# Kernel optimization log

Measured on AMD Instinct MI355X. Metric: run time of the kernel, lower is better.

The kernel has to match this reference:

```python
import jax, jax.numpy as jnp
import numpy as np

K = 3       # kernel_size
STRIDE = 1
PAD = 1


def setup_inputs() -> dict:
    key = jax.random.key(0)
    k1, k2, k3 = jax.random.split(key, 3)
    B, C, H, W = 4, 64, 224, 224
    x = jax.random.normal(k1, (B, C, H, W), dtype=jnp.float32)
    # fc = Conv2d(C, C, 1) -> ReLU -> Conv2d(C, C*K*K, 1); 1x1 convs == per-pixel matmuls
    w1 = jax.random.normal(k2, (C, C), dtype=jnp.float32) * (1.0 / np.sqrt(C))
    w2 = jax.random.normal(k3, (C * K * K, C), dtype=jnp.float32) * (1.0 / np.sqrt(C))
    return {"x": x, "w1": w1, "w2": w2}


def reference(x, w1, w2):
    # Involution-style dynamic depthwise conv:
    # out[b,c,h,w] = sum_{i,j} kern[b,c,i,j,h,w] * x_pad[b,c,h+i,w+j]
    B, C, H, W = x.shape
    # kernel generator (two 1x1 convs with ReLU in between)
    h = jax.nn.relu(jnp.einsum('bchw,oc->bohw', x, w1))
    kern = jnp.einsum('bohw,po->bphw', h, w2).reshape(B, C, K * K, H, W)
    # unfold 3x3 neighborhoods (pad=1, stride=1) -> (B, C, K*K, H, W)
    xp = jnp.pad(x, ((0, 0), (0, 0), (PAD, PAD), (PAD, PAD)))
    patches = jnp.stack(
        [xp[:, :, i:i + H, j:j + W] for i in range(K) for j in range(K)], axis=2)
    return jnp.einsum('bckhw,bckhw->bchw', kern, patches)
```

## Files before the change

### kernel.cpp

```cpp
#include <hip/hip_runtime.h>

#define HH   224
#define WW   224
#define HW_  (HH * WW)
#define TS   16
#define TSH  18
#define NPIX (TSH * TSH)
#define XSR  328

typedef __attribute__((ext_vector_type(8))) short bf16x8;
typedef __attribute__((ext_vector_type(4))) float f32x4;

static __device__ __forceinline__ unsigned short f2bf(float f) {
    unsigned u = __float_as_uint(f);
    u += 0x7FFFu + ((u >> 16) & 1u);
    return (unsigned short)(u >> 16);
}
static __device__ __forceinline__ float bf2f(unsigned short h) {
    return __uint_as_float(((unsigned)h) << 16);
}

__global__ __launch_bounds__(256) void prep_weights(
    const float* __restrict__ w1, const float* __restrict__ w2,
    unsigned short* __restrict__ wsb)
{
    const int i = blockIdx.x * 256 + threadIdx.x;
    unsigned short* w1b = wsb;
    unsigned short* w2p = wsb + 4096;
    if (i < 4096) w1b[i] = f2bf(w1[i]);
    const int c  = i >> 10;
    const int rr = (i >> 6) & 15;
    const int o  = i & 63;
    float v = (rr < 9) ? w2[(c * 9 + rr) * 64 + o] : 0.f;
    w2p[i] = f2bf(v);
}

__global__ __launch_bounds__(256, 2) void dynconv_mfma(
    const float* __restrict__ x, const unsigned short* __restrict__ wsb,
    float* __restrict__ out)
{
    __shared__ __align__(16) unsigned char lds[74752];
    unsigned short* xs  = (unsigned short*)lds;
    unsigned char*  hsb = lds + 41984;

    const unsigned char* w1b = (const unsigned char*)wsb;
    const unsigned char* w2p = (const unsigned char*)(wsb + 4096);

    const int b    = blockIdx.z;
    const int ty0  = blockIdx.y * TS;
    const int tx0  = blockIdx.x * TS;
    const int tid  = threadIdx.x;
    const int lane = tid & 63;
    const int w    = tid >> 6;
    const int tx   = lane & 15;
    const int g    = lane >> 4;

    const float* xb = x + (size_t)b * 64 * HW_;

    for (int i = tid; i < 64 * (NPIX / 2); i += 256) {
        int c  = i / 162;
        int pr = i - c * 162;
        int r  = pr / 9;
        int cp = pr - r * 9;
        int col0 = cp * 2;
        int gy  = ty0 + r - 1;
        int gx0 = tx0 + col0 - 1;
        float f0 = 0.f, f1 = 0.f;
        if ((unsigned)gy < (unsigned)HH) {
            const float* rowp = xb + c * HW_ + gy * WW;
            if ((unsigned)gx0 < (unsigned)WW)       f0 = rowp[gx0];
            if ((unsigned)(gx0 + 1) < (unsigned)WW) f1 = rowp[gx0 + 1];
        }
        unsigned pack = (unsigned)f2bf(f0) | ((unsigned)f2bf(f1) << 16);
        int p0 = r * TSH + col0;
        *(unsigned*)((unsigned char*)xs + c * 656 + p0 * 2) = pack;
    }
    __syncthreads();

    {
        bf16x8 aw1[4][2];
        #pragma unroll
        for (int mt = 0; mt < 4; ++mt) {
            #pragma unroll
            for (int kt = 0; kt < 2; ++kt)
                aw1[mt][kt] = *(const bf16x8*)(w1b + (mt * 16 + tx) * 128 + kt * 64 + g * 16);
        }
        #pragma unroll
        for (int q = 0; q < 4; ++q) {
            const int nt = w * 4 + q;
            const int center = (nt + 1) * TSH + tx + 1;
            bf16x8 bx[2];
            #pragma unroll
            for (int kt = 0; kt < 2; ++kt) {
                bf16x8 t;
                #pragma unroll
                for (int j = 0; j < 8; ++j)
                    t[j] = (short)xs[(kt * 32 + g * 8 + j) * XSR + center];
                bx[kt] = t;
            }
            const int pix = nt * 16 + tx;
            const unsigned swz = (unsigned)((tx & 7) << 4);
            #pragma unroll
            for (int mt = 0; mt < 4; ++mt) {
                f32x4 hc = {0.f, 0.f, 0.f, 0.f};
                hc = __builtin_amdgcn_mfma_f32_16x16x32_bf16(aw1[mt][0], bx[0], hc, 0, 0, 0);
                hc = __builtin_amdgcn_mfma_f32_16x16x32_bf16(aw1[mt][1], bx[1], hc, 0, 0, 0);
                unsigned lo = (unsigned)f2bf(fmaxf(hc[0], 0.f)) | ((unsigned)f2bf(fmaxf(hc[1], 0.f)) << 16);
                unsigned hi = (unsigned)f2bf(fmaxf(hc[2], 0.f)) | ((unsigned)f2bf(fmaxf(hc[3], 0.f)) << 16);
                unsigned byte = ((unsigned)(pix * 128 + mt * 32 + g * 8)) ^ swz;
                *(uint2*)(hsb + byte) = make_uint2(lo, hi);
            }
        }
    }

    bf16x8 bh0[2], bh1[2], bh2[2], bh3[2];
    {
        const unsigned swz = (unsigned)((tx & 7) << 4);
        #pragma unroll
        for (int kt = 0; kt < 2; ++kt) {
            unsigned p0 = (unsigned)(((w * 4 + 0) * 16 + tx) * 128 + kt * 64 + g * 16);
            unsigned p1 = (unsigned)(((w * 4 + 1) * 16 + tx) * 128 + kt * 64 + g * 16);
            unsigned p2 = (unsigned)(((w * 4 + 2) * 16 + tx) * 128 + kt * 64 + g * 16);
            unsigned p3 = (unsigned)(((w * 4 + 3) * 16 + tx) * 128 + kt * 64 + g * 16);
            bh0[kt] = *(const bf16x8*)(hsb + (p0 ^ swz));
            bh1[kt] = *(const bf16x8*)(hsb + (p1 ^ swz));
            bh2[kt] = *(const bf16x8*)(hsb + (p2 ^ swz));
            bh3[kt] = *(const bf16x8*)(hsb + (p3 ^ swz));
        }
    }

    int poff[4][4];
    #pragma unroll
    for (int q = 0; q < 4; ++q) {
        #pragma unroll
        for (int r = 0; r < 4; ++r) {
            int kk = g * 4 + r;
            int kv = kk < 9 ? kk : 0;
            int dy = kv / 3;
            int dx = kv - dy * 3;
            poff[q][r] = (w * 4 + q + dy) * TSH + (tx + dx);
        }
    }

    float* outp = out + (size_t)b * 64 * HW_ + (size_t)(ty0 + w * 4 + g) * WW + tx0 + tx;

    const unsigned char* w2base = w2p + tx * 128 + g * 16;
    bf16x8 na0 = *(const bf16x8*)(w2base);
    bf16x8 na1 = *(const bf16x8*)(w2base + 64);

    for (int c = 0; c < 64; ++c) {
        bf16x8 a0 = na0, a1 = na1;
        const int cn = (c < 63) ? c + 1 : 63;
        na0 = *(const bf16x8*)(w2base + cn * 2048);
        na1 = *(const bf16x8*)(w2base + cn * 2048 + 64);

        f32x4 acc0 = {0.f, 0.f, 0.f, 0.f};
        f32x4 acc1 = {0.f, 0.f, 0.f, 0.f};
        f32x4 acc2 = {0.f, 0.f, 0.f, 0.f};
        f32x4 acc3 = {0.f, 0.f, 0.f, 0.f};
        acc0 = __builtin_amdgcn_mfma_f32_16x16x32_bf16(a0, bh0[0], acc0, 0, 0, 0);
        acc1 = __builtin_amdgcn_mfma_f32_16x16x32_bf16(a0, bh1[0], acc1, 0, 0, 0);
        acc2 = __builtin_amdgcn_mfma_f32_16x16x32_bf16(a0, bh2[0], acc2, 0, 0, 0);
        acc3 = __builtin_amdgcn_mfma_f32_16x16x32_bf16(a0, bh3[0], acc3, 0, 0, 0);
        acc0 = __builtin_amdgcn_mfma_f32_16x16x32_bf16(a1, bh0[1], acc0, 0, 0, 0);
        acc1 = __builtin_amdgcn_mfma_f32_16x16x32_bf16(a1, bh1[1], acc1, 0, 0, 0);
        acc2 = __builtin_amdgcn_mfma_f32_16x16x32_bf16(a1, bh2[1], acc2, 0, 0, 0);
        acc3 = __builtin_amdgcn_mfma_f32_16x16x32_bf16(a1, bh3[1], acc3, 0, 0, 0);

        const unsigned short* xc = xs + c * XSR;
        float part0 = 0.f, part1 = 0.f, part2 = 0.f, part3 = 0.f;
        #pragma unroll
        for (int r = 0; r < 4; ++r) {
            part0 = fmaf(acc0[r], bf2f(xc[poff[0][r]]), part0);
            part1 = fmaf(acc1[r], bf2f(xc[poff[1][r]]), part1);
            part2 = fmaf(acc2[r], bf2f(xc[poff[2][r]]), part2);
            part3 = fmaf(acc3[r], bf2f(xc[poff[3][r]]), part3);
        }
        part0 += __shfl_xor(part0, 16, 64); part0 += __shfl_xor(part0, 32, 64);
        part1 += __shfl_xor(part1, 16, 64); part1 += __shfl_xor(part1, 32, 64);
        part2 += __shfl_xor(part2, 16, 64); part2 += __shfl_xor(part2, 32, 64);
        part3 += __shfl_xor(part3, 16, 64); part3 += __shfl_xor(part3, 32, 64);

        float v = part0;
        v = (g == 1) ? part1 : v;
        v = (g == 2) ? part2 : v;
        v = (g == 3) ? part3 : v;
        outp[(size_t)c * HW_] = v;
    }
}

extern "C" void kernel_launch(void* const* d_in, const int* in_sizes, int n_in,
                              void* d_out, int out_size, void* d_ws, size_t ws_size,
                              hipStream_t stream) {
    (void)in_sizes; (void)n_in; (void)out_size; (void)ws_size;
    const float* x  = (const float*)d_in[0];
    const float* w1 = (const float*)d_in[1];
    const float* w2 = (const float*)d_in[2];
    float* out = (float*)d_out;
    unsigned short* wsb = (unsigned short*)d_ws;

    prep_weights<<<256, 256, 0, stream>>>(w1, w2, wsb);

    dim3 grid(WW / TS, HH / TS, 4);
    dynconv_mfma<<<grid, 256, 0, stream>>>(x, wsb, out);
}
```

Before: 213.9 us.

## Keep hidden activations in registers via 16x16x16 MFMA and pixel-major LDS layout

```diff
diff --git a/kernel.cpp b/kernel.cpp
--- a/kernel.cpp
+++ b/kernel.cpp
@@ -6,9 +6,10 @@
 #define TS   16
 #define TSH  18
 #define NPIX (TSH * TSH)
-#define XSR  328
+#define XROW 144
 
 typedef __attribute__((ext_vector_type(8))) short bf16x8;
+typedef __attribute__((ext_vector_type(4))) short bf16x4;
 typedef __attribute__((ext_vector_type(4))) float f32x4;
 
 static __device__ __forceinline__ unsigned short f2bf(float f) {
@@ -35,13 +36,11 @@
     w2p[i] = f2bf(v);
 }
 
-__global__ __launch_bounds__(256, 2) void dynconv_mfma(
+__global__ __launch_bounds__(256, 3) void dynconv_mfma16(
     const float* __restrict__ x, const unsigned short* __restrict__ wsb,
     float* __restrict__ out)
 {
-    __shared__ __align__(16) unsigned char lds[74752];
-    unsigned short* xs  = (unsigned short*)lds;
-    unsigned char*  hsb = lds + 41984;
+    __shared__ __align__(16) unsigned char xsb[NPIX * XROW];
 
     const unsigned char* w1b = (const unsigned char*)wsb;
     const unsigned char* w2p = (const unsigned char*)(wsb + 4096);
@@ -57,81 +56,54 @@
 
     const float* xb = x + (size_t)b * 64 * HW_;
 
-    for (int i = tid; i < 64 * (NPIX / 2); i += 256) {
-        int c  = i / 162;
-        int pr = i - c * 162;
-        int r  = pr / 9;
-        int cp = pr - r * 9;
-        int col0 = cp * 2;
+    for (int i = tid; i < 32 * NPIX; i += 256) {
+        int cp  = i / NPIX;
+        int pix = i - cp * NPIX;
+        int r   = pix / TSH;
+        int col = pix - r * TSH;
         int gy  = ty0 + r - 1;
-        int gx0 = tx0 + col0 - 1;
+        int gx  = tx0 + col - 1;
         float f0 = 0.f, f1 = 0.f;
-        if ((unsigned)gy < (unsigned)HH) {
-            const float* rowp = xb + c * HW_ + gy * WW;
-            if ((unsigned)gx0 < (unsigned)WW)       f0 = rowp[gx0];
-            if ((unsigned)(gx0 + 1) < (unsigned)WW) f1 = rowp[gx0 + 1];
+        if ((unsigned)gy < (unsigned)HH && (unsigned)gx < (unsigned)WW) {
+            const float* p = xb + (size_t)(2 * cp) * HW_ + gy * WW + gx;
+            f0 = p[0];
+            f1 = p[HW_];
         }
-        unsigned pack = (unsigned)f2bf(f0) | ((unsigned)f2bf(f1) << 16);
-        int p0 = r * TSH + col0;
-        *(unsigned*)((unsigned char*)xs + c * 656 + p0 * 2) = pack;
+        unsigned pk = (unsigned)f2bf(f0) | ((unsigned)f2bf(f1) << 16);
+        *(unsigned*)(xsb + pix * XROW + cp * 4) = pk;
     }
     __syncthreads();
 
+    bf16x4 bq[4][4];
     {
         bf16x8 aw1[4][2];
         #pragma unroll
-        for (int mt = 0; mt < 4; ++mt) {
+        for (int mt = 0; mt < 4; ++mt)
             #pragma unroll
             for (int kt = 0; kt < 2; ++kt)
                 aw1[mt][kt] = *(const bf16x8*)(w1b + (mt * 16 + tx) * 128 + kt * 64 + g * 16);
-        }
         #pragma unroll
         for (int q = 0; q < 4; ++q) {
-            const int nt = w * 4 + q;
-            const int center = (nt + 1) * TSH + tx + 1;
-            bf16x8 bx[2];
-            #pragma unroll
-            for (int kt = 0; kt < 2; ++kt) {
-                bf16x8 t;
-                #pragma unroll
-                for (int j = 0; j < 8; ++j)
-                    t[j] = (short)xs[(kt * 32 + g * 8 + j) * XSR + center];
-                bx[kt] = t;
-            }
-            const int pix = nt * 16 + tx;
-            const unsigned swz = (unsigned)((tx & 7) << 4);
+            const int center = (w * 4 + q + 1) * TSH + (tx + 1);
+            bf16x8 bx0 = *(const bf16x8*)(xsb + center * XROW + g * 16);
+            bf16x8 bx1 = *(const bf16x8*)(xsb + center * XROW + 64 + g * 16);
             #pragma unroll
             for (int mt = 0; mt < 4; ++mt) {
                 f32x4 hc = {0.f, 0.f, 0.f, 0.f};
-                hc = __builtin_amdgcn_mfma_f32_16x16x32_bf16(aw1[mt][0], bx[0], hc, 0, 0, 0);
-                hc = __builtin_amdgcn_mfma_f32_16x16x32_bf16(aw1[mt][1], bx[1], hc, 0, 0, 0);
+                hc = __builtin_amdgcn_mfma_f32_16x16x32_bf16(aw1[mt][0], bx0, hc, 0, 0, 0);
+                hc = __builtin_amdgcn_mfma_f32_16x16x32_bf16(aw1[mt][1], bx1, hc, 0, 0, 0);
                 unsigned lo = (unsigned)f2bf(fmaxf(hc[0], 0.f)) | ((unsigned)f2bf(fmaxf(hc[1], 0.f)) << 16);
                 unsigned hi = (unsigned)f2bf(fmaxf(hc[2], 0.f)) | ((unsigned)f2bf(fmaxf(hc[3], 0.f)) << 16);
-                unsigned byte = ((unsigned)(pix * 128 + mt * 32 + g * 8)) ^ swz;
-                *(uint2*)(hsb + byte) = make_uint2(lo, hi);
+                union { uint2 u; bf16x4 v; } cv;
+                cv.u = make_uint2(lo, hi);
+                bq[q][mt] = cv.v;
             }
-        }
-    }
-
-    bf16x8 bh0[2], bh1[2], bh2[2], bh3[2];
-    {
-        const unsigned swz = (unsigned)((tx & 7) << 4);
-        #pragma unroll
-        for (int kt = 0; kt < 2; ++kt) {
-            unsigned p0 = (unsigned)(((w * 4 + 0) * 16 + tx) * 128 + kt * 64 + g * 16);
-            unsigned p1 = (unsigned)(((w * 4 + 1) * 16 + tx) * 128 + kt * 64 + g * 16);
-            unsigned p2 = (unsigned)(((w * 4 + 2) * 16 + tx) * 128 + kt * 64 + g * 16);
-            unsigned p3 = (unsigned)(((w * 4 + 3) * 16 + tx) * 128 + kt * 64 + g * 16);
-            bh0[kt] = *(const bf16x8*)(hsb + (p0 ^ swz));
-            bh1[kt] = *(const bf16x8*)(hsb + (p1 ^ swz));
-            bh2[kt] = *(const bf16x8*)(hsb + (p2 ^ swz));
-            bh3[kt] = *(const bf16x8*)(hsb + (p3 ^ swz));
         }
     }
 
     int poff[4][4];
     #pragma unroll
-    for (int q = 0; q < 4; ++q) {
+    for (int q = 0; q < 4; ++q)
         #pragma unroll
         for (int r = 0; r < 4; ++r) {
             int kk = g * 4 + r;
@@ -140,52 +112,71 @@
             int dx = kv - dy * 3;
             poff[q][r] = (w * 4 + q + dy) * TSH + (tx + dx);
         }
-    }
 
     float* outp = out + (size_t)b * 64 * HW_ + (size_t)(ty0 + w * 4 + g) * WW + tx0 + tx;
 
-    const unsigned char* w2base = w2p + tx * 128 + g * 16;
-    bf16x8 na0 = *(const bf16x8*)(w2base);
-    bf16x8 na1 = *(const bf16x8*)(w2base + 64);
+    const unsigned char* w2l = w2p + tx * 128 + g * 8;
+    uint2 pf0[4], pf1[4];
+    #pragma unroll
+    for (int kb = 0; kb < 4; ++kb) {
+        pf0[kb] = *(const uint2*)(w2l + kb * 32);
+        pf1[kb] = *(const uint2*)(w2l + 2048 + kb * 32);
+    }
 
-    for (int c = 0; c < 64; ++c) {
-        bf16x8 a0 = na0, a1 = na1;
-        const int cn = (c < 63) ? c + 1 : 63;
-        na0 = *(const bf16x8*)(w2base + cn * 2048);
-        na1 = *(const bf16x8*)(w2base + cn * 2048 + 64);
+    for (int c = 0; c < 64; c += 2) {
+        union { uint2 u; bf16x4 v; } a2A[4], a2B[4];
+        #pragma unroll
+        for (int kb = 0; kb < 4; ++kb) { a2A[kb].u = pf0[kb]; a2B[kb].u = pf1[kb]; }
+        const int cn = (c + 2 < 64) ? c + 2 : 62;
+        #pragma unroll
+        for (int kb = 0; kb < 4; ++kb) {
+            pf0[kb] = *(const uint2*)(w2l + cn * 2048 + kb * 32);
+            pf1[kb] = *(const uint2*)(w2l + (cn + 1) * 2048 + kb * 32);
+        }
 
-        f32x4 acc0 = {0.f, 0.f, 0.f, 0.f};
-        f32x4 acc1 = {0.f, 0.f, 0.f, 0.f};
-        f32x4 acc2 = {0.f, 0.f, 0.f, 0.f};
-        f32x4 acc3 = {0.f, 0.f, 0.f, 0.f};
-        acc0 = __builtin_amdgcn_mfma_f32_16x16x32_bf16(a0, bh0[0], acc0, 0, 0, 0);
-        acc1 = __builtin_amdgcn_mfma_f32_16x16x32_bf16(a0, bh1[0], acc1, 0, 0, 0);
-        acc2 = __builtin_amdgcn_mfma_f32_16x16x32_bf16(a0, bh2[0], acc2, 0, 0, 0);
-        acc3 = __builtin_amdgcn_mfma_f32_16x16x32_bf16(a0, bh3[0], acc3, 0, 0, 0);
-        acc0 = __builtin_amdgcn_mfma_f32_16x16x32_bf16(a1, bh0[1], acc0, 0, 0, 0);
-        acc1 = __builtin_amdgcn_mfma_f32_16x16x32_bf16(a1, bh1[1], acc1, 0, 0, 0);
-        acc2 = __builtin_amdgcn_mfma_f32_16x16x32_bf16(a1, bh2[1], acc2, 0, 0, 0);
-        acc3 = __builtin_amdgcn_mfma_f32_16x16x32_bf16(a1, bh3[1], acc3, 0, 0, 0);
+        f32x4 accA[4], accB[4];
+        #pragma unroll
+        for (int q = 0; q < 4; ++q) {
+            accA[q] = f32x4{0.f, 0.f, 0.f, 0.f};
+            accB[q] = f32x4{0.f, 0.f, 0.f, 0.f};
+        }
+        #pragma unroll
+        for (int kb = 0; kb < 4; ++kb)
+            #pragma unroll
+            for (int q = 0; q < 4; ++q)
+                accA[q] = __builtin_amdgcn_mfma_f32_16x16x16bf16_1k(a2A[kb].v, bq[q][kb], accA[q], 0, 0, 0);
+        #pragma unroll
+        for (int kb = 0; kb < 4; ++kb)
+            #pragma unroll
+            for (int q = 0; q < 4; ++q)
+                accB[q] = __builtin_amdgcn_mfma_f32_16x16x16bf16_1k(a2B[kb].v, bq[q][kb], accB[q], 0, 0, 0);
 
-        const unsigned short* xc = xs + c * XSR;
-        float part0 = 0.f, part1 = 0.f, part2 = 0.f, part3 = 0.f;
+        unsigned pp[4][4];
         #pragma unroll
-        for (int r = 0; r < 4; ++r) {
-            part0 = fmaf(acc0[r], bf2f(xc[poff[0][r]]), part0);
-            part1 = fmaf(acc1[r], bf2f(xc[poff[1][r]]), part1);
-            part2 = fmaf(acc2[r], bf2f(xc[poff[2][r]]), part2);
-            part3 = fmaf(acc3[r], bf2f(xc[poff[3][r]]), part3);
+        for (int q = 0; q < 4; ++q)
+            #pragma unroll
+            for (int r = 0; r < 4; ++r)
+                pp[q][r] = *(const unsigned*)(xsb + poff[q][r] * XROW + c * 2);
+
+        float pt[4], pu[4];
+        #pragma unroll
+        for (int q = 0; q < 4; ++q) {
+            float s = 0.f, t = 0.f;
+            #pragma unroll
+            for (int r = 0; r < 4; ++r) {
+                s = fmaf(accA[q][r], __uint_as_float(pp[q][r] << 16), s);
+                t = fmaf(accB[q][r], __uint_as_float(pp[q][r] & 0xffff0000u), t);
+            }
+            s += __shfl_xor(s, 16, 64); s += __shfl_xor(s, 32, 64);
+            t += __shfl_xor(t, 16, 64); t += __shfl_xor(t, 32, 64);
+            pt[q] = s; pu[q] = t;
         }
-        part0 += __shfl_xor(part0, 16, 64); part0 += __shfl_xor(part0, 32, 64);
-        part1 += __shfl_xor(part1, 16, 64); part1 += __shfl_xor(part1, 32, 64);
-        part2 += __shfl_xor(part2, 16, 64); part2 += __shfl_xor(part2, 32, 64);
-        part3 += __shfl_xor(part3, 16, 64); part3 += __shfl_xor(part3, 32, 64);
-
-        float v = part0;
-        v = (g == 1) ? part1 : v;
-        v = (g == 2) ? part2 : v;
-        v = (g == 3) ? part3 : v;
-        outp[(size_t)c * HW_] = v;
+        float vA = pt[0];
+        vA = (g == 1) ? pt[1] : vA; vA = (g == 2) ? pt[2] : vA; vA = (g == 3) ? pt[3] : vA;
+        float vB = pu[0];
+        vB = (g == 1) ? pu[1] : vB; vB = (g == 2) ? pu[2] : vB; vB = (g == 3) ? pu[3] : vB;
+        outp[(size_t)c * HW_] = vA;
+        outp[(size_t)(c + 1) * HW_] = vB;
     }
 }
 
@@ -202,5 +193,5 @@
     prep_weights<<<256, 256, 0, stream>>>(w1, w2, wsb);
 
     dim3 grid(WW / TS, HH / TS, 4);
-    dynconv_mfma<<<grid, 256, 0, stream>>>(x, wsb, out);
+    dynconv_mfma16<<<grid, 256, 0, stream>>>(x, wsb, out);
 }
```

Measured after the change: 248.1 us. 1.16x slower.

## Shrink tile to 16x8, keep hidden activations in registers via 16x16x16 MFMA

Applied to the files above, without the earlier changes.

```diff
diff --git a/kernel.cpp b/kernel.cpp
--- a/kernel.cpp
+++ b/kernel.cpp
@@ -3,12 +3,14 @@
 #define HH   224
 #define WW   224
 #define HW_  (HH * WW)
-#define TS   16
-#define TSH  18
-#define NPIX (TSH * TSH)
-#define XSR  328
+#define TW   16
+#define TH   8
+#define HLW  18
+#define HLH  10
+#define XSR  184
 
 typedef __attribute__((ext_vector_type(8))) short bf16x8;
+typedef __attribute__((ext_vector_type(4))) short bf16x4;
 typedef __attribute__((ext_vector_type(4))) float f32x4;
 
 static __device__ __forceinline__ unsigned short f2bf(float f) {
@@ -35,20 +37,18 @@
     w2p[i] = f2bf(v);
 }
 
-__global__ __launch_bounds__(256, 2) void dynconv_mfma(
+__global__ __launch_bounds__(256, 6) void dynconv_mfma16(
     const float* __restrict__ x, const unsigned short* __restrict__ wsb,
     float* __restrict__ out)
 {
-    __shared__ __align__(16) unsigned char lds[74752];
-    unsigned short* xs  = (unsigned short*)lds;
-    unsigned char*  hsb = lds + 41984;
+    __shared__ __align__(16) unsigned short xs[64 * XSR];
 
     const unsigned char* w1b = (const unsigned char*)wsb;
     const unsigned char* w2p = (const unsigned char*)(wsb + 4096);
 
     const int b    = blockIdx.z;
-    const int ty0  = blockIdx.y * TS;
-    const int tx0  = blockIdx.x * TS;
+    const int ty0  = blockIdx.y * TH;
+    const int tx0  = blockIdx.x * TW;
     const int tid  = threadIdx.x;
     const int lane = tid & 63;
     const int w    = tid >> 6;
@@ -57,38 +57,36 @@
 
     const float* xb = x + (size_t)b * 64 * HW_;
 
-    for (int i = tid; i < 64 * (NPIX / 2); i += 256) {
-        int c  = i / 162;
-        int pr = i - c * 162;
-        int r  = pr / 9;
-        int cp = pr - r * 9;
+    for (int i = tid; i < 64 * 90; i += 256) {
+        int c    = i / 90;
+        int rem  = i - c * 90;
+        int r    = rem / 9;
+        int cp   = rem - r * 9;
         int col0 = cp * 2;
-        int gy  = ty0 + r - 1;
-        int gx0 = tx0 + col0 - 1;
+        int gy   = ty0 + r - 1;
+        int gx0  = tx0 + col0 - 1;
         float f0 = 0.f, f1 = 0.f;
         if ((unsigned)gy < (unsigned)HH) {
             const float* rowp = xb + c * HW_ + gy * WW;
             if ((unsigned)gx0 < (unsigned)WW)       f0 = rowp[gx0];
             if ((unsigned)(gx0 + 1) < (unsigned)WW) f1 = rowp[gx0 + 1];
         }
-        unsigned pack = (unsigned)f2bf(f0) | ((unsigned)f2bf(f1) << 16);
-        int p0 = r * TSH + col0;
-        *(unsigned*)((unsigned char*)xs + c * 656 + p0 * 2) = pack;
+        unsigned pk = (unsigned)f2bf(f0) | ((unsigned)f2bf(f1) << 16);
+        *(unsigned*)((unsigned char*)xs + c * 368 + (r * HLW + col0) * 2) = pk;
     }
     __syncthreads();
 
+    bf16x4 bq[2][4];
     {
         bf16x8 aw1[4][2];
         #pragma unroll
-        for (int mt = 0; mt < 4; ++mt) {
+        for (int mt = 0; mt < 4; ++mt)
             #pragma unroll
             for (int kt = 0; kt < 2; ++kt)
                 aw1[mt][kt] = *(const bf16x8*)(w1b + (mt * 16 + tx) * 128 + kt * 64 + g * 16);
-        }
         #pragma unroll
-        for (int q = 0; q < 4; ++q) {
-            const int nt = w * 4 + q;
-            const int center = (nt + 1) * TSH + tx + 1;
+        for (int q = 0; q < 2; ++q) {
+            const int center = (w * 2 + q + 1) * HLW + (tx + 1);
             bf16x8 bx[2];
             #pragma unroll
             for (int kt = 0; kt < 2; ++kt) {
@@ -98,8 +96,6 @@
                     t[j] = (short)xs[(kt * 32 + g * 8 + j) * XSR + center];
                 bx[kt] = t;
             }
-            const int pix = nt * 16 + tx;
-            const unsigned swz = (unsigned)((tx & 7) << 4);
             #pragma unroll
             for (int mt = 0; mt < 4; ++mt) {
                 f32x4 hc = {0.f, 0.f, 0.f, 0.f};
@@ -107,85 +103,63 @@
                 hc = __builtin_amdgcn_mfma_f32_16x16x32_bf16(aw1[mt][1], bx[1], hc, 0, 0, 0);
                 unsigned lo = (unsigned)f2bf(fmaxf(hc[0], 0.f)) | ((unsigned)f2bf(fmaxf(hc[1], 0.f)) << 16);
                 unsigned hi = (unsigned)f2bf(fmaxf(hc[2], 0.f)) | ((unsigned)f2bf(fmaxf(hc[3], 0.f)) << 16);
-                unsigned byte = ((unsigned)(pix * 128 + mt * 32 + g * 8)) ^ swz;
-                *(uint2*)(hsb + byte) = make_uint2(lo, hi);
+                union { uint2 u; bf16x4 v; } cv;
+                cv.u = make_uint2(lo, hi);
+                bq[q][mt] = cv.v;
             }
         }
     }
 
-    bf16x8 bh0[2], bh1[2], bh2[2], bh3[2];
-    {
-        const unsigned swz = (unsigned)((tx & 7) << 4);
-        #pragma unroll
-        for (int kt = 0; kt < 2; ++kt) {
-            unsigned p0 = (unsigned)(((w * 4 + 0) * 16 + tx) * 128 + kt * 64 + g * 16);
-            unsigned p1 = (unsigned)(((w * 4 + 1) * 16 + tx) * 128 + kt * 64 + g * 16);
-            unsigned p2 = (unsigned)(((w * 4 + 2) * 16 + tx) * 128 + kt * 64 + g * 16);
-            unsigned p3 = (unsigned)(((w * 4 + 3) * 16 + tx) * 128 + kt * 64 + g * 16);
-            bh0[kt] = *(const bf16x8*)(hsb + (p0 ^ swz));
-            bh1[kt] = *(const bf16x8*)(hsb + (p1 ^ swz));
-            bh2[kt] = *(const bf16x8*)(hsb + (p2 ^ swz));
-            bh3[kt] = *(const bf16x8*)(hsb + (p3 ^ swz));
-        }
-    }
-
-    int poff[4][4];
+    int poff[2][4];
     #pragma unroll
-    for (int q = 0; q < 4; ++q) {
+    for (int q = 0; q < 2; ++q)
         #pragma unroll
         for (int r = 0; r < 4; ++r) {
             int kk = g * 4 + r;
             int kv = kk < 9 ? kk : 0;
             int dy = kv / 3;
             int dx = kv - dy * 3;
-            poff[q][r] = (w * 4 + q + dy) * TSH + (tx + dx);
+            poff[q][r] = (w * 2 + q + dy) * HLW + (tx + dx);
         }
-    }
 
-    float* outp = out + (size_t)b * 64 * HW_ + (size_t)(ty0 + w * 4 + g) * WW + tx0 + tx;
+    const int orow = ty0 + w * 2 + g;
+    float* outp = out + (size_t)b * 64 * HW_ + (size_t)orow * WW + tx0 + tx;
 
-    const unsigned char* w2base = w2p + tx * 128 + g * 16;
-    bf16x8 na0 = *(const bf16x8*)(w2base);
-    bf16x8 na1 = *(const bf16x8*)(w2base + 64);
+    const unsigned char* w2l = w2p + tx * 128 + g * 8;
+    uint2 pf[4];
+    #pragma unroll
+    for (int kb = 0; kb < 4; ++kb) pf[kb] = *(const uint2*)(w2l + kb * 32);
 
     for (int c = 0; c < 64; ++c) {
-        bf16x8 a0 = na0, a1 = na1;
+        union { uint2 u; bf16x4 v; } a2[4];
+        #pragma unroll
+        for (int kb = 0; kb < 4; ++kb) a2[kb].u = pf[kb];
         const int cn = (c < 63) ? c + 1 : 63;
-        na0 = *(const bf16x8*)(w2base + cn * 2048);
-        na1 = *(const bf16x8*)(w2base + cn * 2048 + 64);
+        #pragma unroll
+        for (int kb = 0; kb < 4; ++kb) pf[kb] = *(const uint2*)(w2l + cn * 2048 + kb * 32);
 
         f32x4 acc0 = {0.f, 0.f, 0.f, 0.f};
         f32x4 acc1 = {0.f, 0.f, 0.f, 0.f};
-        f32x4 acc2 = {0.f, 0.f, 0.f, 0.f};
-        f32x4 acc3 = {0.f, 0.f, 0.f, 0.f};
-        acc0 = __builtin_amdgcn_mfma_f32_16x16x32_bf16(a0, bh0[0], acc0, 0, 0, 0);
-        acc1 = __builtin_amdgcn_mfma_f32_16x16x32_bf16(a0, bh1[0], acc1, 0, 0, 0);
-        acc2 = __builtin_amdgcn_mfma_f32_16x16x32_bf16(a0, bh2[0], acc2, 0, 0, 0);
-        acc3 = __builtin_amdgcn_mfma_f32_16x16x32_bf16(a0, bh3[0], acc3, 0, 0, 0);
-        acc0 = __builtin_amdgcn_mfma_f32_16x16x32_bf16(a1, bh0[1], acc0, 0, 0, 0);
-        acc1 = __builtin_amdgcn_mfma_f32_16x16x32_bf16(a1, bh1[1], acc1, 0, 0, 0);
-        acc2 = __builtin_amdgcn_mfma_f32_16x16x32_bf16(a1, bh2[1], acc2, 0, 0, 0);
-        acc3 = __builtin_amdgcn_mfma_f32_16x16x32_bf16(a1, bh3[1], acc3, 0, 0, 0);
+        #pragma unroll
+        for (int kb = 0; kb < 4; ++kb) {
+            acc0 = __builtin_amdgcn_mfma_f32_16x16x16bf16_1k(a2[kb].v, bq[0][kb], acc0, 0, 0, 0);
+            acc1 = __builtin_amdgcn_mfma_f32_16x16x16bf16_1k(a2[kb].v, bq[1][kb], acc1, 0, 0, 0);
+        }
 
         const unsigned short* xc = xs + c * XSR;
-        float part0 = 0.f, part1 = 0.f, part2 = 0.f, part3 = 0.f;
+        float s0 = 0.f, s1 = 0.f;
         #pragma unroll
         for (int r = 0; r < 4; ++r) {
-            part0 = fmaf(acc0[r], bf2f(xc[poff[0][r]]), part0);
-            part1 = fmaf(acc1[r], bf2f(xc[poff[1][r]]), part1);
-            part2 = fmaf(acc2[r], bf2f(xc[poff[2][r]]), part2);
-            part3 = fmaf(acc3[r], bf2f(xc[poff[3][r]]), part3);
+            s0 = fmaf(acc0[r], bf2f(xc[poff[0][r]]), s0);
+            s1 = fmaf(acc1[r], bf2f(xc[poff[1][r]]), s1);
         }
-        part0 += __shfl_xor(part0, 16, 64); part0 += __shfl_xor(part0, 32, 64);
-        part1 += __shfl_xor(part1, 16, 64); part1 += __shfl_xor(part1, 32, 64);
-        part2 += __shfl_xor(part2, 16, 64); part2 += __shfl_xor(part2, 32, 64);
-        part3 += __shfl_xor(part3, 16, 64); part3 += __shfl_xor(part3, 32, 64);
+        s0 += __shfl_xor(s0, 16, 64); s0 += __shfl_xor(s0, 32, 64);
+        s1 += __shfl_xor(s1, 16, 64); s1 += __shfl_xor(s1, 32, 64);
 
-        float v = part0;
-        v = (g == 1) ? part1 : v;
-        v = (g == 2) ? part2 : v;
-        v = (g == 3) ? part3 : v;
-        outp[(size_t)c * HW_] = v;
+        if (g < 2) {
+            float v = (g == 0) ? s0 : s1;
+            outp[(size_t)c * HW_] = v;
+        }
     }
 }
 
@@ -201,6 +175,6 @@
 
     prep_weights<<<256, 256, 0, stream>>>(w1, w2, wsb);
 
-    dim3 grid(WW / TS, HH / TS, 4);
-    dynconv_mfma<<<grid, 256, 0, stream>>>(x, wsb, out);
+    dim3 grid(WW / TW, HH / TH, 4);
+    dynconv_mfma16<<<grid, 256, 0, stream>>>(x, wsb, out);
 }
```

New measurement: 321.4 us. +50.3%, slower.
